# Performance work log

Measured on AMD Instinct MI355X. Metric: run time of the kernel, lower is better.

The kernel has to match this reference:

```python
import jax, jax.numpy as jnp
import numpy as np

BINS = 128
POOL = 4  # AdaptiveAvgPool3d(4) output size


def _resize_axis(a, axis, out_size):
    """1D linear resize along `axis`, matching torch trilinear align_corners=False."""
    in_size = a.shape[axis]
    scale = in_size / out_size
    coords = (jnp.arange(out_size, dtype=a.dtype) + 0.5) * scale - 0.5
    coords = jnp.clip(coords, 0.0, in_size - 1)
    lo = jnp.floor(coords).astype(jnp.int32)
    hi = jnp.minimum(lo + 1, in_size - 1)
    w = coords - lo.astype(a.dtype)
    shape = [1] * a.ndim
    shape[axis] = out_size
    w = w.reshape(shape)
    a_lo = jnp.take(a, lo, axis=axis)
    a_hi = jnp.take(a, hi, axis=axis)
    return a_lo * (1.0 - w) + a_hi * w


def setup_inputs() -> dict:
    key = jax.random.key(0)
    k1, k2, k3 = jax.random.split(key, 3)
    B, C, D, H, W = 2, 64, 64, 64, 64
    Cm = C // 8  # channels // reduction
    x = jax.random.normal(k1, (B, C, D, H, W), jnp.float32)
    w1 = jax.random.normal(k2, (Cm, C), jnp.float32) * 0.1   # Conv3d 1x1, no bias
    w2 = jax.random.normal(k3, (1, Cm), jnp.float32) * 0.1   # Conv3d 1x1, no bias
    return {"x": x, "w1": w1, "w2": w2}


def reference(x, w1, w2):
    B, C, D, H, W = x.shape
    # AdaptiveAvgPool3d(4): D,H,W divisible by 4 -> exact block means
    p = x.reshape(B, C, POOL, D // POOL, POOL, H // POOL, POOL, W // POOL)
    p = p.mean(axis=(3, 5, 7))  # (B, C, 4, 4, 4)
    # 1x1x1 conv == channel contraction
    h = jnp.einsum('oc,bcdhw->bodhw', w1, p)  # (B, Cm, 4, 4, 4)
    # InstanceNorm3d (affine=False), per (B, channel) over spatial dims
    mu = h.mean(axis=(2, 3, 4), keepdims=True)
    var = h.var(axis=(2, 3, 4), keepdims=True)
    h = (h - mu) / jnp.sqrt(var + 1e-5)
    h = jax.nn.gelu(h, approximate=False)  # torch nn.GELU default = exact erf
    s = jax.nn.sigmoid(jnp.einsum('oc,bcdhw->bodhw', w2, h))  # (B, 1, 4, 4, 4)
    # trilinear upsample (align_corners=False), separable per axis
    for axis, size in ((2, D), (3, H), (4, W)):
        s = _resize_axis(s, axis, size)
    weighted = x * s  # broadcast over channels
    x_min = weighted.min()
    x_max = weighted.max()
    x_norm = (weighted - x_min) / (x_max - x_min + 1e-8)
    # torch.histc(bins=BINS, min=0, max=1): values in [0,1]; v==1 -> last bin
    idx = jnp.clip(jnp.floor(x_norm.reshape(-1) * BINS).astype(jnp.int32), 0, BINS - 1)
    hist = jnp.zeros((BINS,), x.dtype).at[idx].add(1.0)
    prob = hist / (hist.sum() + 1e-10)
    entropy = -jnp.sum(prob * jnp.log2(prob + 1e-10))
    return entropy
```

## Files before the change

### kernel.cpp

```cpp
#include <hip/hip_runtime.h>
#include <math.h>

#define BINS 128


__device__ __forceinline__ unsigned mapf(float f) {
    unsigned u = __float_as_uint(f);
    return (u & 0x80000000u) ? ~u : (u | 0x80000000u);
}
__device__ __forceinline__ float unmapf(unsigned m) {
    unsigned u = (m & 0x80000000u) ? (m & 0x7FFFFFFFu) : ~m;
    return __uint_as_float(u);
}
__device__ __forceinline__ float sel4(float g0, float g1, float g2, float g3, int k) {
    float a = (k & 1) ? g1 : g0;
    float b = (k & 1) ? g3 : g2;
    return (k & 2) ? b : a;
}
__device__ __forceinline__ void axgate(int v, int& lo, int& hi, float& fr) {
    float c = ((float)v + 0.5f) * 0.0625f - 0.5f;
    c = fminf(fmaxf(c, 0.0f), 3.0f);
    int l = (int)floorf(c);
    lo = l; hi = min(l + 1, 3); fr = c - (float)l;
}

__global__ __launch_bounds__(256) void pool_kernel(const float* __restrict__ x,
                                                   float* __restrict__ p) {
    const int blk = blockIdx.x;
    const int t = threadIdx.x;
    const float4* xb = (const float4*)x + (size_t)blk * 16384;
    float acc0 = 0.f, acc1 = 0.f, acc2 = 0.f, acc3 = 0.f;
    for (int n = 0; n < 64; n += 4) {
        float4 v0 = xb[(n + 0) * 256 + t]; acc0 += (v0.x + v0.y) + (v0.z + v0.w);
        float4 v1 = xb[(n + 1) * 256 + t]; acc1 += (v1.x + v1.y) + (v1.z + v1.w);
        float4 v2 = xb[(n + 2) * 256 + t]; acc2 += (v2.x + v2.y) + (v2.z + v2.w);
        float4 v3 = xb[(n + 3) * 256 + t]; acc3 += (v3.x + v3.y) + (v3.z + v3.w);
    }
    #pragma unroll
    for (int m = 0; m < 4; ++m) {
        int mask = (m == 0) ? 1 : (m == 1) ? 2 : (m == 2) ? 16 : 32;
        acc0 += __shfl_xor(acc0, mask);
        acc1 += __shfl_xor(acc1, mask);
        acc2 += __shfl_xor(acc2, mask);
        acc3 += __shfl_xor(acc3, mask);
    }
    __shared__ float red[64];
    const int lane = t & 63, wave = t >> 6;
    if (lane < 16 && (lane & 3) == 0) {
        const int pw = lane >> 2;
        red[(0 * 4 + pw) * 4 + wave] = acc0;
        red[(1 * 4 + pw) * 4 + wave] = acc1;
        red[(2 * 4 + pw) * 4 + wave] = acc2;
        red[(3 * 4 + pw) * 4 + wave] = acc3;
    }
    __syncthreads();
    if (t < 16)
        p[blk * 16 + t] = (red[t * 4 + 0] + red[t * 4 + 1] + red[t * 4 + 2] + red[t * 4 + 3]) * (1.0f / 4096.0f);
}

__global__ __launch_bounds__(1024) void mid_kernel(const float* __restrict__ p,
                                                   const float* __restrict__ w1,
                                                   const float* __restrict__ w2,
                                                   float* __restrict__ s_out,
                                                   unsigned* __restrict__ mm,
                                                   unsigned* __restrict__ hist) {
    __shared__ float hs[2 * 8 * 64];
    const int t = threadIdx.x;
    const int b = t >> 9, cm = (t >> 6) & 7, sp = t & 63;
    float h = 0.f;
    const float* pb = p + b * 64 * 64 + sp;
    const float* w1r = w1 + cm * 64;
    for (int c = 0; c < 64; ++c) h += w1r[c] * pb[c * 64];
    float s1 = h;
    #pragma unroll
    for (int m = 1; m <= 32; m <<= 1) s1 += __shfl_xor(s1, m);
    const float mu = s1 * (1.0f / 64.0f);
    float d = h - mu;
    float s2 = d * d;
    #pragma unroll
    for (int m = 1; m <= 32; m <<= 1) s2 += __shfl_xor(s2, m);
    const float var = s2 * (1.0f / 64.0f);
    const float hn = d / sqrtf(var + 1e-5f);
    hs[(b * 8 + cm) * 64 + sp] = 0.5f * hn * (1.0f + erff(hn * 0.70710678118654752440f));
    __syncthreads();
    if (t < 128) {
        const int bb = t >> 6, ss = t & 63;
        float acc = 0.f;
        #pragma unroll
        for (int c = 0; c < 8; ++c) acc += w2[c] * hs[(bb * 8 + c) * 64 + ss];
        s_out[t] = 1.0f / (1.0f + expf(-acc));
    }
    if (t == 0) { mm[0] = 0xFFFFFFFFu; mm[1] = 0u; }
    if (t >= 128 && t < 256) hist[t - 128] = 0u;
}


#define PASS_SETUP2()                                                                 \
    const int t = threadIdx.x;                                                        \
    const int bid = blockIdx.x;                                                       \
    const int cbase = (bid & 7) * 256 + (bid >> 3) * 4;                               \
    const int b = cbase >> 10;                                                        \
    if (t < 64) ls64[t] = s[b * 64 + t];                                              \
    int wl0, wh0, wl1, wh1, wl2, wh2, wl3, wh3;                                       \
    float fw0, fw1, fw2, fw3;                                                         \
    {                                                                                 \
        const int wb = (t & 15) * 4;                                                  \
        axgate(wb + 0, wl0, wh0, fw0); axgate(wb + 1, wl1, wh1, fw1);                 \
        axgate(wb + 2, wl2, wh2, fw2); axgate(wb + 3, wl3, wh3, fw3);                 \
    }                                                                                 \
    const int rbase = t >> 4;                                                         \
    __syncthreads();                                                                  \
    _Pragma("unroll")                                                                 \
    for (int k = 0; k < 4; ++k) {                                                     \
        const int e = k * 256 + t;                                                    \
        const int dloc = e >> 6, hh_ = e & 63;                                        \
        int dl, dh2; float fd; axgate((cbase & 15) * 4 + dloc, dl, dh2, fd);          \
        int hl, hh3; float fh; axgate(hh_, hl, hh3, fh);                              \
        const float w00 = (1.f - fd) * (1.f - fh), w01 = (1.f - fd) * fh;             \
        const float w10 = fd * (1.f - fh), w11 = fd * fh;                             \
        const int i00 = dl * 16 + hl * 4, i01 = dl * 16 + hh3 * 4;                    \
        const int i10 = dh2 * 16 + hl * 4, i11 = dh2 * 16 + hh3 * 4;                  \
        rowg[e] = make_float4(                                                        \
            w00 * ls64[i00 + 0] + w01 * ls64[i01 + 0] + w10 * ls64[i10 + 0] + w11 * ls64[i11 + 0], \
            w00 * ls64[i00 + 1] + w01 * ls64[i01 + 1] + w10 * ls64[i10 + 1] + w11 * ls64[i11 + 1], \
            w00 * ls64[i00 + 2] + w01 * ls64[i01 + 2] + w10 * ls64[i10 + 2] + w11 * ls64[i11 + 2], \
            w00 * ls64[i00 + 3] + w01 * ls64[i01 + 3] + w10 * ls64[i10 + 3] + w11 * ls64[i11 + 3]);\
    }                                                                                 \
    __syncthreads();

#define LOADS16(IT)                                                                   \
    const float4* xp = (const float4*)x + (size_t)(cbase + (IT)) * 4096;              \
    const float4 u0  = xp[ 0*256+t], u1  = xp[ 1*256+t], u2  = xp[ 2*256+t], u3  = xp[ 3*256+t]; \
    const float4 u4  = xp[ 4*256+t], u5  = xp[ 5*256+t], u6  = xp[ 6*256+t], u7  = xp[ 7*256+t]; \
    const float4 u8  = xp[ 8*256+t], u9  = xp[ 9*256+t], u10 = xp[10*256+t], u11 = xp[11*256+t]; \
    const float4 u12 = xp[12*256+t], u13 = xp[13*256+t], u14 = xp[14*256+t], u15 = xp[15*256+t]; \
    __builtin_amdgcn_sched_barrier(0);

#define GATE4A(IT, K, G0, G1, G2, G3)                                                 \
    float G0, G1, G2, G3;                                                             \
    {                                                                                 \
        float4 rg = rowg[(IT) * 256 + (K) * 16 + rbase];                              \
        float lo, hi;                                                                 \
        lo = sel4(rg.x, rg.y, rg.z, rg.w, wl0); hi = sel4(rg.x, rg.y, rg.z, rg.w, wh0); G0 = lo + fw0 * (hi - lo); \
        lo = sel4(rg.x, rg.y, rg.z, rg.w, wl1); hi = sel4(rg.x, rg.y, rg.z, rg.w, wh1); G1 = lo + fw1 * (hi - lo); \
        lo = sel4(rg.x, rg.y, rg.z, rg.w, wl2); hi = sel4(rg.x, rg.y, rg.z, rg.w, wh2); G2 = lo + fw2 * (hi - lo); \
        lo = sel4(rg.x, rg.y, rg.z, rg.w, wl3); hi = sel4(rg.x, rg.y, rg.z, rg.w, wh3); G3 = lo + fw3 * (hi - lo); \
    }

__global__ __launch_bounds__(256) void gated_minmax_kernel(const float* __restrict__ x,
                                                           const float* __restrict__ s,
                                                           unsigned* __restrict__ mm) {
    __shared__ float ls64[64];
    __shared__ float4 rowg[1024];
    __shared__ float red[8];
    PASS_SETUP2()

    float vmin = INFINITY, vmax = -INFINITY;
    #pragma unroll
    for (int it = 0; it < 4; ++it) {
        LOADS16(it)
#define MM1(K, U)                                                                     \
        {                                                                             \
            GATE4A(it, K, g0, g1, g2, g3);                                            \
            float p0 = U.x * g0, p1 = U.y * g1, p2 = U.z * g2, p3 = U.w * g3;         \
            vmin = fminf(vmin, fminf(fminf(p0, p1), fminf(p2, p3)));                  \
            vmax = fmaxf(vmax, fmaxf(fmaxf(p0, p1), fmaxf(p2, p3)));                  \
        }
        MM1(0,u0) MM1(1,u1) MM1(2,u2) MM1(3,u3) MM1(4,u4) MM1(5,u5) MM1(6,u6) MM1(7,u7)
        MM1(8,u8) MM1(9,u9) MM1(10,u10) MM1(11,u11) MM1(12,u12) MM1(13,u13) MM1(14,u14) MM1(15,u15)
#undef MM1
    }

    #pragma unroll
    for (int m = 1; m <= 32; m <<= 1) {
        vmin = fminf(vmin, __shfl_xor(vmin, m));
        vmax = fmaxf(vmax, __shfl_xor(vmax, m));
    }
    const int wave = t >> 6;
    __syncthreads();
    if ((t & 63) == 0) { red[wave] = vmin; red[4 + wave] = vmax; }
    __syncthreads();
    if (t == 0) {
        float m0 = fminf(fminf(red[0], red[1]), fminf(red[2], red[3]));
        float M0 = fmaxf(fmaxf(red[4], red[5]), fmaxf(red[6], red[7]));
        atomicMin(&mm[0], mapf(m0));
        atomicMax(&mm[1], mapf(M0));
    }
}

__global__ __launch_bounds__(256) void gated_hist_kernel(const float* __restrict__ x,
                                                         const float* __restrict__ s,
                                                         const unsigned* __restrict__ mm,
                                                         unsigned* __restrict__ ghist) {
    __shared__ float ls64[64];
    __shared__ float4 rowg[1024];
    __shared__ unsigned lh[BINS];
    if (threadIdx.x < BINS) lh[threadIdx.x] = 0u;
    PASS_SETUP2()

    const float vmin = unmapf(mm[0]);
    const float vmax = unmapf(mm[1]);
    const float inv = 128.0f / (vmax - vmin + 1e-8f);

    #pragma unroll
    for (int it = 0; it < 4; ++it) {
        LOADS16(it)
#define PKK(K, U)                                                                     \
        unsigned pk##K;                                                               \
        {                                                                             \
            GATE4A(it, K, g0, g1, g2, g3);                                            \
            float p0 = U.x * g0, p1 = U.y * g1, p2 = U.z * g2, p3 = U.w * g3;         \
            int i0 = (int)floorf((p0 - vmin) * inv);                                  \
            int i1 = (int)floorf((p1 - vmin) * inv);                                  \
            int i2 = (int)floorf((p2 - vmin) * inv);                                  \
            int i3 = (int)floorf((p3 - vmin) * inv);                                  \
            i0 = min(max(i0, 0), BINS - 1); i1 = min(max(i1, 0), BINS - 1);           \
            i2 = min(max(i2, 0), BINS - 1); i3 = min(max(i3, 0), BINS - 1);           \
            pk##K = (unsigned)i0 | ((unsigned)i1 << 8) |                              \
                    ((unsigned)i2 << 16) | ((unsigned)i3 << 24);                      \
        }
        PKK(0,u0) PKK(1,u1) PKK(2,u2) PKK(3,u3) PKK(4,u4) PKK(5,u5) PKK(6,u6) PKK(7,u7)
        PKK(8,u8) PKK(9,u9) PKK(10,u10) PKK(11,u11) PKK(12,u12) PKK(13,u13) PKK(14,u14) PKK(15,u15)
#undef PKK
        __builtin_amdgcn_sched_barrier(0);
#define AT(K)                                                                         \
        atomicAdd(&lh[pk##K & 255u], 1u);                                             \
        atomicAdd(&lh[(pk##K >> 8) & 255u], 1u);                                      \
        atomicAdd(&lh[(pk##K >> 16) & 255u], 1u);                                     \
        atomicAdd(&lh[pk##K >> 24], 1u);
        AT(0) AT(1) AT(2) AT(3) AT(4) AT(5) AT(6) AT(7)
        AT(8) AT(9) AT(10) AT(11) AT(12) AT(13) AT(14) AT(15)
#undef AT
        __builtin_amdgcn_sched_barrier(0);
    }

    __syncthreads();
    if (t < BINS) {
        unsigned c = lh[t];
        if (c) atomicAdd(&ghist[t], c);
    }
}

__global__ __launch_bounds__(64) void entropy_kernel(const unsigned* __restrict__ ghist,
                                                     float* __restrict__ out) {
    const int t = threadIdx.x;
    float c0 = (float)ghist[t];
    float c1 = (float)ghist[t + 64];
    float s = c0 + c1;
    #pragma unroll
    for (int m = 1; m <= 32; m <<= 1) s += __shfl_xor(s, m);
    const float inv = 1.0f / (s + 1e-10f);
    float p0 = c0 * inv, p1 = c1 * inv;
    float e = p0 * log2f(p0 + 1e-10f) + p1 * log2f(p1 + 1e-10f);
    #pragma unroll
    for (int m = 1; m <= 32; m <<= 1) e += __shfl_xor(e, m);
    if (t == 0) out[0] = -e;
}

extern "C" void kernel_launch(void* const* d_in, const int* in_sizes, int n_in,
                              void* d_out, int out_size, void* d_ws, size_t ws_size,
                              hipStream_t stream) {
    (void)in_sizes; (void)n_in; (void)out_size; (void)ws_size;
    const float* x  = (const float*)d_in[0];
    const float* w1 = (const float*)d_in[1];
    const float* w2 = (const float*)d_in[2];
    float* out = (float*)d_out;
    float* ws  = (float*)d_ws;

    float* p        = ws;
    float* s        = ws + 8192;
    unsigned* mm    = (unsigned*)(ws + 8448);
    unsigned* hist  = (unsigned*)(ws + 8456);

    pool_kernel<<<512, 256, 0, stream>>>(x, p);
    mid_kernel<<<1, 1024, 0, stream>>>(p, w1, w2, s, mm, hist);
    gated_minmax_kernel<<<512, 256, 0, stream>>>(x, s, mm);
    gated_hist_kernel<<<512, 256, 0, stream>>>(x, s, mm, hist);
    entropy_kernel<<<1, 64, 0, stream>>>(hist, out);
}
```

Measured before the change: 96.12 us.

## Fuse min/max, histogram and entropy kernels with a software grid barrier

Merges the gated min/max pass, the histogram pass and the entropy kernel into one persistent 512-block kernel. A global atomic barrier separates the min/max reduction from the histogram phase, and a completion counter lets block 0 compute the entropy. This removes two kernel launches and the repeated per-block gate-table setup. It also replaces the select-based trilinear gate with a 4-weight dot product and folds the bin index into one FMA. The grid barrier assumes all 512 blocks are co-resident, and the FMA index without floor may round differently at bin edges.

```diff
diff --git a/kernel.cpp b/kernel.cpp
--- a/kernel.cpp
+++ b/kernel.cpp
@@ -11,17 +11,28 @@
 __device__ __forceinline__ float unmapf(unsigned m) {
     unsigned u = (m & 0x80000000u) ? (m & 0x7FFFFFFFu) : ~m;
     return __uint_as_float(u);
-}
-__device__ __forceinline__ float sel4(float g0, float g1, float g2, float g3, int k) {
-    float a = (k & 1) ? g1 : g0;
-    float b = (k & 1) ? g3 : g2;
-    return (k & 2) ? b : a;
 }
 __device__ __forceinline__ void axgate(int v, int& lo, int& hi, float& fr) {
     float c = ((float)v + 0.5f) * 0.0625f - 0.5f;
     c = fminf(fmaxf(c, 0.0f), 3.0f);
     int l = (int)floorf(c);
     lo = l; hi = min(l + 1, 3); fr = c - (float)l;
+}
+
+__device__ __forceinline__ void gbar(unsigned* bar, unsigned* gen, unsigned nb) {
+    __syncthreads();
+    if (threadIdx.x == 0) {
+        __threadfence();
+        unsigned g = atomicAdd(gen, 0u);
+        if (atomicAdd(bar, 1u) == nb - 1u) {
+            atomicExch(bar, 0u);
+            __threadfence();
+            atomicAdd(gen, 1u);
+        } else {
+            while (atomicAdd(gen, 0u) == g) __builtin_amdgcn_s_sleep(4);
+        }
+    }
+    __syncthreads();
 }
 
 __global__ __launch_bounds__(256) void pool_kernel(const float* __restrict__ x,
@@ -63,7 +74,8 @@
                                                    const float* __restrict__ w2,
                                                    float* __restrict__ s_out,
                                                    unsigned* __restrict__ mm,
-                                                   unsigned* __restrict__ hist) {
+                                                   unsigned* __restrict__ hist,
+                                                   unsigned* __restrict__ barv) {
     __shared__ float hs[2 * 8 * 64];
     const int t = threadIdx.x;
     const int b = t >> 9, cm = (t >> 6) & 7, sp = t & 63;
@@ -90,42 +102,62 @@
         for (int c = 0; c < 8; ++c) acc += w2[c] * hs[(bb * 8 + c) * 64 + ss];
         s_out[t] = 1.0f / (1.0f + expf(-acc));
     }
-    if (t == 0) { mm[0] = 0xFFFFFFFFu; mm[1] = 0u; }
+    if (t == 0) {
+        mm[0] = 0xFFFFFFFFu; mm[1] = 0u;
+        barv[0] = 0u; barv[1] = 0u; barv[2] = 0u;
+    }
     if (t >= 128 && t < 256) hist[t - 128] = 0u;
 }
 
-
-#define PASS_SETUP2()                                                                 \
-    const int t = threadIdx.x;                                                        \
-    const int bid = blockIdx.x;                                                       \
-    const int cbase = (bid & 7) * 256 + (bid >> 3) * 4;                               \
-    const int b = cbase >> 10;                                                        \
-    if (t < 64) ls64[t] = s[b * 64 + t];                                              \
-    int wl0, wh0, wl1, wh1, wl2, wh2, wl3, wh3;                                       \
-    float fw0, fw1, fw2, fw3;                                                         \
-    {                                                                                 \
-        const int wb = (t & 15) * 4;                                                  \
-        axgate(wb + 0, wl0, wh0, fw0); axgate(wb + 1, wl1, wh1, fw1);                 \
-        axgate(wb + 2, wl2, wh2, fw2); axgate(wb + 3, wl3, wh3, fw3);                 \
-    }                                                                                 \
-    const int rbase = t >> 4;                                                         \
-    __syncthreads();                                                                  \
-    _Pragma("unroll")                                                                 \
-    for (int k = 0; k < 4; ++k) {                                                     \
-        const int e = k * 256 + t;                                                    \
-        const int dloc = e >> 6, hh_ = e & 63;                                        \
-        int dl, dh2; float fd; axgate((cbase & 15) * 4 + dloc, dl, dh2, fd);          \
-        int hl, hh3; float fh; axgate(hh_, hl, hh3, fh);                              \
-        const float w00 = (1.f - fd) * (1.f - fh), w01 = (1.f - fd) * fh;             \
-        const float w10 = fd * (1.f - fh), w11 = fd * fh;                             \
-        const int i00 = dl * 16 + hl * 4, i01 = dl * 16 + hh3 * 4;                    \
-        const int i10 = dh2 * 16 + hl * 4, i11 = dh2 * 16 + hh3 * 4;                  \
-        rowg[e] = make_float4(                                                        \
-            w00 * ls64[i00 + 0] + w01 * ls64[i01 + 0] + w10 * ls64[i10 + 0] + w11 * ls64[i11 + 0], \
-            w00 * ls64[i00 + 1] + w01 * ls64[i01 + 1] + w10 * ls64[i10 + 1] + w11 * ls64[i11 + 1], \
-            w00 * ls64[i00 + 2] + w01 * ls64[i01 + 2] + w10 * ls64[i10 + 2] + w11 * ls64[i11 + 2], \
-            w00 * ls64[i00 + 3] + w01 * ls64[i01 + 3] + w10 * ls64[i10 + 3] + w11 * ls64[i11 + 3]);\
-    }                                                                                 \
+__global__ __launch_bounds__(256) void fused_mmh_kernel(const float* __restrict__ x,
+                                                        const float* __restrict__ s,
+                                                        unsigned* __restrict__ mm,
+                                                        unsigned* __restrict__ ghist,
+                                                        unsigned* __restrict__ barv,
+                                                        float* __restrict__ out) {
+    __shared__ float ls64[64];
+    __shared__ float4 rowg[1024];
+    __shared__ unsigned lh[BINS];
+    __shared__ float red[8];
+    const int t = threadIdx.x;
+    const int bid = blockIdx.x;
+    const int cbase = (bid & 7) * 256 + (bid >> 3) * 4;
+    const int b = cbase >> 10;
+    if (t < 64) ls64[t] = s[b * 64 + t];
+    if (t < BINS) lh[t] = 0u;
+
+    float4 wva, wvb, wvc, wvd;
+    {
+        const int wb = (t & 15) * 4;
+        #define MKWV(WV, J)                                                           \
+        {                                                                             \
+            int lo, hi; float fr; axgate(wb + (J), lo, hi, fr);                       \
+            const float om = 1.0f - fr;                                               \
+            WV.x = (lo == 0 ? om : 0.f) + (hi == 0 ? fr : 0.f);                       \
+            WV.y = (lo == 1 ? om : 0.f) + (hi == 1 ? fr : 0.f);                       \
+            WV.z = (lo == 2 ? om : 0.f) + (hi == 2 ? fr : 0.f);                       \
+            WV.w = (lo == 3 ? om : 0.f) + (hi == 3 ? fr : 0.f);                       \
+        }
+        MKWV(wva, 0) MKWV(wvb, 1) MKWV(wvc, 2) MKWV(wvd, 3)
+        #undef MKWV
+    }
+    const int rbase = t >> 4;
+    __syncthreads();
+    #pragma unroll
+    for (int k = 0; k < 4; ++k) {
+        const int e = k * 256 + t;
+        int dl, dh2; float fd; axgate((cbase & 15) * 4 + (e >> 6), dl, dh2, fd);
+        int hl, hh3; float fh; axgate(e & 63, hl, hh3, fh);
+        const float w00 = (1.f - fd) * (1.f - fh), w01 = (1.f - fd) * fh;
+        const float w10 = fd * (1.f - fh), w11 = fd * fh;
+        const int i00 = dl * 16 + hl * 4, i01 = dl * 16 + hh3 * 4;
+        const int i10 = dh2 * 16 + hl * 4, i11 = dh2 * 16 + hh3 * 4;
+        rowg[e] = make_float4(
+            w00 * ls64[i00 + 0] + w01 * ls64[i01 + 0] + w10 * ls64[i10 + 0] + w11 * ls64[i11 + 0],
+            w00 * ls64[i00 + 1] + w01 * ls64[i01 + 1] + w10 * ls64[i10 + 1] + w11 * ls64[i11 + 1],
+            w00 * ls64[i00 + 2] + w01 * ls64[i01 + 2] + w10 * ls64[i10 + 2] + w11 * ls64[i11 + 2],
+            w00 * ls64[i00 + 3] + w01 * ls64[i01 + 3] + w10 * ls64[i10 + 3] + w11 * ls64[i11 + 3]);
+    }
     __syncthreads();
 
 #define LOADS16(IT)                                                                   \
@@ -136,71 +168,59 @@
     const float4 u12 = xp[12*256+t], u13 = xp[13*256+t], u14 = xp[14*256+t], u15 = xp[15*256+t]; \
     __builtin_amdgcn_sched_barrier(0);
 
-#define GATE4A(IT, K, G0, G1, G2, G3)                                                 \
+#define GATE4W(IT, K, G0, G1, G2, G3)                                                 \
     float G0, G1, G2, G3;                                                             \
     {                                                                                 \
         float4 rg = rowg[(IT) * 256 + (K) * 16 + rbase];                              \
-        float lo, hi;                                                                 \
-        lo = sel4(rg.x, rg.y, rg.z, rg.w, wl0); hi = sel4(rg.x, rg.y, rg.z, rg.w, wh0); G0 = lo + fw0 * (hi - lo); \
-        lo = sel4(rg.x, rg.y, rg.z, rg.w, wl1); hi = sel4(rg.x, rg.y, rg.z, rg.w, wh1); G1 = lo + fw1 * (hi - lo); \
-        lo = sel4(rg.x, rg.y, rg.z, rg.w, wl2); hi = sel4(rg.x, rg.y, rg.z, rg.w, wh2); G2 = lo + fw2 * (hi - lo); \
-        lo = sel4(rg.x, rg.y, rg.z, rg.w, wl3); hi = sel4(rg.x, rg.y, rg.z, rg.w, wh3); G3 = lo + fw3 * (hi - lo); \
-    }
-
-__global__ __launch_bounds__(256) void gated_minmax_kernel(const float* __restrict__ x,
-                                                           const float* __restrict__ s,
-                                                           unsigned* __restrict__ mm) {
-    __shared__ float ls64[64];
-    __shared__ float4 rowg[1024];
-    __shared__ float red[8];
-    PASS_SETUP2()
-
-    float vmin = INFINITY, vmax = -INFINITY;
-    #pragma unroll
-    for (int it = 0; it < 4; ++it) {
-        LOADS16(it)
+        G0 = rg.x * wva.x + rg.y * wva.y + rg.z * wva.z + rg.w * wva.w;               \
+        G1 = rg.x * wvb.x + rg.y * wvb.y + rg.z * wvb.z + rg.w * wvb.w;               \
+        G2 = rg.x * wvc.x + rg.y * wvc.y + rg.z * wvc.z + rg.w * wvc.w;               \
+        G3 = rg.x * wvd.x + rg.y * wvd.y + rg.z * wvd.z + rg.w * wvd.w;               \
+    }
+
+    {
+        float vmin = INFINITY, vmax = -INFINITY;
+        #pragma unroll
+        for (int it = 0; it < 4; ++it) {
+            LOADS16(it)
 #define MM1(K, U)                                                                     \
-        {                                                                             \
-            GATE4A(it, K, g0, g1, g2, g3);                                            \
-            float p0 = U.x * g0, p1 = U.y * g1, p2 = U.z * g2, p3 = U.w * g3;         \
-            vmin = fminf(vmin, fminf(fminf(p0, p1), fminf(p2, p3)));                  \
-            vmax = fmaxf(vmax, fmaxf(fmaxf(p0, p1), fmaxf(p2, p3)));                  \
-        }
-        MM1(0,u0) MM1(1,u1) MM1(2,u2) MM1(3,u3) MM1(4,u4) MM1(5,u5) MM1(6,u6) MM1(7,u7)
-        MM1(8,u8) MM1(9,u9) MM1(10,u10) MM1(11,u11) MM1(12,u12) MM1(13,u13) MM1(14,u14) MM1(15,u15)
+            {                                                                         \
+                GATE4W(it, K, g0, g1, g2, g3);                                        \
+                float p0 = U.x * g0, p1 = U.y * g1, p2 = U.z * g2, p3 = U.w * g3;     \
+                vmin = fminf(vmin, fminf(fminf(p0, p1), fminf(p2, p3)));              \
+                vmax = fmaxf(vmax, fmaxf(fmaxf(p0, p1), fmaxf(p2, p3)));              \
+            }
+            MM1(0,u0) MM1(1,u1) MM1(2,u2) MM1(3,u3) MM1(4,u4) MM1(5,u5) MM1(6,u6) MM1(7,u7)
+            MM1(8,u8) MM1(9,u9) MM1(10,u10) MM1(11,u11) MM1(12,u12) MM1(13,u13) MM1(14,u14) MM1(15,u15)
 #undef MM1
-    }
-
-    #pragma unroll
-    for (int m = 1; m <= 32; m <<= 1) {
-        vmin = fminf(vmin, __shfl_xor(vmin, m));
-        vmax = fmaxf(vmax, __shfl_xor(vmax, m));
-    }
-    const int wave = t >> 6;
-    __syncthreads();
-    if ((t & 63) == 0) { red[wave] = vmin; red[4 + wave] = vmax; }
-    __syncthreads();
+        }
+        #pragma unroll
+        for (int m = 1; m <= 32; m <<= 1) {
+            vmin = fminf(vmin, __shfl_xor(vmin, m));
+            vmax = fmaxf(vmax, __shfl_xor(vmax, m));
+        }
+        const int wave = t >> 6;
+        __syncthreads();
+        if ((t & 63) == 0) { red[wave] = vmin; red[4 + wave] = vmax; }
+        __syncthreads();
+        if (t == 0) {
+            float m0 = fminf(fminf(red[0], red[1]), fminf(red[2], red[3]));
+            float M0 = fmaxf(fmaxf(red[4], red[5]), fmaxf(red[6], red[7]));
+            atomicMin(&mm[0], mapf(m0));
+            atomicMax(&mm[1], mapf(M0));
+        }
+    }
+
+    gbar(&barv[0], &barv[1], 512u);
+
     if (t == 0) {
-        float m0 = fminf(fminf(red[0], red[1]), fminf(red[2], red[3]));
-        float M0 = fmaxf(fmaxf(red[4], red[5]), fmaxf(red[6], red[7]));
-        atomicMin(&mm[0], mapf(m0));
-        atomicMax(&mm[1], mapf(M0));
-    }
-}
-
-__global__ __launch_bounds__(256) void gated_hist_kernel(const float* __restrict__ x,
-                                                         const float* __restrict__ s,
-                                                         const unsigned* __restrict__ mm,
-                                                         unsigned* __restrict__ ghist) {
-    __shared__ float ls64[64];
-    __shared__ float4 rowg[1024];
-    __shared__ unsigned lh[BINS];
-    if (threadIdx.x < BINS) lh[threadIdx.x] = 0u;
-    PASS_SETUP2()
-
-    const float vmin = unmapf(mm[0]);
-    const float vmax = unmapf(mm[1]);
-    const float inv = 128.0f / (vmax - vmin + 1e-8f);
+        red[0] = unmapf(atomicAdd(&mm[0], 0u));
+        red[1] = unmapf(atomicAdd(&mm[1], 0u));
+    }
+    __syncthreads();
+    const float vmn = red[0];
+    const float inv = 128.0f / (red[1] - vmn + 1e-8f);
+    const float nvm = -vmn * inv;
 
     #pragma unroll
     for (int it = 0; it < 4; ++it) {
@@ -208,12 +228,12 @@
 #define PKK(K, U)                                                                     \
         unsigned pk##K;                                                               \
         {                                                                             \
-            GATE4A(it, K, g0, g1, g2, g3);                                            \
+            GATE4W(it, K, g0, g1, g2, g3);                                            \
             float p0 = U.x * g0, p1 = U.y * g1, p2 = U.z * g2, p3 = U.w * g3;         \
-            int i0 = (int)floorf((p0 - vmin) * inv);                                  \
-            int i1 = (int)floorf((p1 - vmin) * inv);                                  \
-            int i2 = (int)floorf((p2 - vmin) * inv);                                  \
-            int i3 = (int)floorf((p3 - vmin) * inv);                                  \
+            int i0 = (int)(p0 * inv + nvm);                                           \
+            int i1 = (int)(p1 * inv + nvm);                                           \
+            int i2 = (int)(p2 * inv + nvm);                                           \
+            int i3 = (int)(p3 * inv + nvm);                                           \
             i0 = min(max(i0, 0), BINS - 1); i1 = min(max(i1, 0), BINS - 1);           \
             i2 = min(max(i2, 0), BINS - 1); i3 = min(max(i3, 0), BINS - 1);           \
             pk##K = (unsigned)i0 | ((unsigned)i1 << 8) |                              \
@@ -233,28 +253,35 @@
 #undef AT
         __builtin_amdgcn_sched_barrier(0);
     }
-
     __syncthreads();
     if (t < BINS) {
         unsigned c = lh[t];
         if (c) atomicAdd(&ghist[t], c);
     }
-}
-
-__global__ __launch_bounds__(64) void entropy_kernel(const unsigned* __restrict__ ghist,
-                                                     float* __restrict__ out) {
-    const int t = threadIdx.x;
-    float c0 = (float)ghist[t];
-    float c1 = (float)ghist[t + 64];
-    float s = c0 + c1;
-    #pragma unroll
-    for (int m = 1; m <= 32; m <<= 1) s += __shfl_xor(s, m);
-    const float inv = 1.0f / (s + 1e-10f);
-    float p0 = c0 * inv, p1 = c1 * inv;
-    float e = p0 * log2f(p0 + 1e-10f) + p1 * log2f(p1 + 1e-10f);
-    #pragma unroll
-    for (int m = 1; m <= 32; m <<= 1) e += __shfl_xor(e, m);
-    if (t == 0) out[0] = -e;
+    __syncthreads();
+    if (t == 0) { __threadfence(); atomicAdd(&barv[2], 1u); }
+
+    if (bid == 0) {
+        if (t == 0) {
+            while (atomicAdd(&barv[2], 0u) < 512u) __builtin_amdgcn_s_sleep(4);
+        }
+        __syncthreads();
+        if (t < 64) {
+            float c0 = (float)atomicAdd(&ghist[t], 0u);
+            float c1 = (float)atomicAdd(&ghist[t + 64], 0u);
+            float ssum = c0 + c1;
+            #pragma unroll
+            for (int m = 1; m <= 32; m <<= 1) ssum += __shfl_xor(ssum, m);
+            const float is = 1.0f / (ssum + 1e-10f);
+            float p0 = c0 * is, p1 = c1 * is;
+            float e = p0 * log2f(p0 + 1e-10f) + p1 * log2f(p1 + 1e-10f);
+            #pragma unroll
+            for (int m = 1; m <= 32; m <<= 1) e += __shfl_xor(e, m);
+            if (t == 0) out[0] = -e;
+        }
+    }
+#undef LOADS16
+#undef GATE4W
 }
 
 extern "C" void kernel_launch(void* const* d_in, const int* in_sizes, int n_in,
@@ -270,11 +297,10 @@
     float* p        = ws;
     float* s        = ws + 8192;
     unsigned* mm    = (unsigned*)(ws + 8448);
+    unsigned* barv  = (unsigned*)(ws + 8450);
     unsigned* hist  = (unsigned*)(ws + 8456);
 
     pool_kernel<<<512, 256, 0, stream>>>(x, p);
-    mid_kernel<<<1, 1024, 0, stream>>>(p, w1, w2, s, mm, hist);
-    gated_minmax_kernel<<<512, 256, 0, stream>>>(x, s, mm);
-    gated_hist_kernel<<<512, 256, 0, stream>>>(x, s, mm, hist);
-    entropy_kernel<<<1, 64, 0, stream>>>(hist, out);
-}
+    mid_kernel<<<1, 1024, 0, stream>>>(p, w1, w2, s, mm, hist, barv);
+    fused_mmh_kernel<<<512, 256, 0, stream>>>(x, s, mm, hist, barv, out);
+}
```

Measured after the change: 152.6 us. 1.59x slower.

## Replace select-based W-gate interpolation with weight dot products and simplify streaming loops

Applied to the files above, without the earlier changes.

The per-thread W-axis interpolation now uses precomputed 4-wide weight vectors and a dot product instead of sel4 selects and a lerp. The 16-load batched blocks with sched_barriers are replaced by a single 64-iteration loop unrolled by 4, leaving load scheduling to the compiler. In the histogram pass the bin index becomes a fused multiply-add with truncation instead of a subtract, multiply and floorf, and atomics are issued right after each element. Fewer loads in flight could reduce memory-level parallelism, and truncation differs from floor for slightly negative values, but the clamp to zero covers that.

```diff
diff --git a/kernel.cpp b/kernel.cpp
--- a/kernel.cpp
+++ b/kernel.cpp
@@ -11,11 +11,6 @@
 __device__ __forceinline__ float unmapf(unsigned m) {
     unsigned u = (m & 0x80000000u) ? (m & 0x7FFFFFFFu) : ~m;
     return __uint_as_float(u);
-}
-__device__ __forceinline__ float sel4(float g0, float g1, float g2, float g3, int k) {
-    float a = (k & 1) ? g1 : g0;
-    float b = (k & 1) ? g3 : g2;
-    return (k & 2) ? b : a;
 }
 __device__ __forceinline__ void axgate(int v, int& lo, int& hi, float& fr) {
     float c = ((float)v + 0.5f) * 0.0625f - 0.5f;
@@ -95,27 +90,36 @@
 }
 
 
-#define PASS_SETUP2()                                                                 \
+#define PASS_SETUP4()                                                                 \
     const int t = threadIdx.x;                                                        \
     const int bid = blockIdx.x;                                                       \
     const int cbase = (bid & 7) * 256 + (bid >> 3) * 4;                               \
     const int b = cbase >> 10;                                                        \
     if (t < 64) ls64[t] = s[b * 64 + t];                                              \
-    int wl0, wh0, wl1, wh1, wl2, wh2, wl3, wh3;                                       \
-    float fw0, fw1, fw2, fw3;                                                         \
+    float4 wva, wvb, wvc, wvd;      \
     {                                                                                 \
         const int wb = (t & 15) * 4;                                                  \
-        axgate(wb + 0, wl0, wh0, fw0); axgate(wb + 1, wl1, wh1, fw1);                 \
-        axgate(wb + 2, wl2, wh2, fw2); axgate(wb + 3, wl3, wh3, fw3);                 \
+        int lo, hi; float fr, om;                                                     \
+        axgate(wb + 0, lo, hi, fr); om = 1.0f - fr;                                   \
+        wva = make_float4((lo==0?om:0.f)+(hi==0?fr:0.f), (lo==1?om:0.f)+(hi==1?fr:0.f),\
+                          (lo==2?om:0.f)+(hi==2?fr:0.f), (lo==3?om:0.f)+(hi==3?fr:0.f));\
+        axgate(wb + 1, lo, hi, fr); om = 1.0f - fr;                                   \
+        wvb = make_float4((lo==0?om:0.f)+(hi==0?fr:0.f), (lo==1?om:0.f)+(hi==1?fr:0.f),\
+                          (lo==2?om:0.f)+(hi==2?fr:0.f), (lo==3?om:0.f)+(hi==3?fr:0.f));\
+        axgate(wb + 2, lo, hi, fr); om = 1.0f - fr;                                   \
+        wvc = make_float4((lo==0?om:0.f)+(hi==0?fr:0.f), (lo==1?om:0.f)+(hi==1?fr:0.f),\
+                          (lo==2?om:0.f)+(hi==2?fr:0.f), (lo==3?om:0.f)+(hi==3?fr:0.f));\
+        axgate(wb + 3, lo, hi, fr); om = 1.0f - fr;                                   \
+        wvd = make_float4((lo==0?om:0.f)+(hi==0?fr:0.f), (lo==1?om:0.f)+(hi==1?fr:0.f),\
+                          (lo==2?om:0.f)+(hi==2?fr:0.f), (lo==3?om:0.f)+(hi==3?fr:0.f));\
     }                                                                                 \
     const int rbase = t >> 4;                                                         \
     __syncthreads();                                                                  \
     _Pragma("unroll")                                                                 \
-    for (int k = 0; k < 4; ++k) {                                                     \
+    for (int k = 0; k < 4; ++k) {             \
         const int e = k * 256 + t;                                                    \
-        const int dloc = e >> 6, hh_ = e & 63;                                        \
-        int dl, dh2; float fd; axgate((cbase & 15) * 4 + dloc, dl, dh2, fd);          \
-        int hl, hh3; float fh; axgate(hh_, hl, hh3, fh);                              \
+        int dl, dh2; float fd; axgate((cbase & 15) * 4 + (e >> 6), dl, dh2, fd);      \
+        int hl, hh3; float fh; axgate(e & 63, hl, hh3, fh);                           \
         const float w00 = (1.f - fd) * (1.f - fh), w01 = (1.f - fd) * fh;             \
         const float w10 = fd * (1.f - fh), w11 = fd * fh;                             \
         const int i00 = dl * 16 + hl * 4, i01 = dl * 16 + hh3 * 4;                    \
@@ -126,25 +130,17 @@
             w00 * ls64[i00 + 2] + w01 * ls64[i01 + 2] + w10 * ls64[i10 + 2] + w11 * ls64[i11 + 2], \
             w00 * ls64[i00 + 3] + w01 * ls64[i01 + 3] + w10 * ls64[i10 + 3] + w11 * ls64[i11 + 3]);\
     }                                                                                 \
-    __syncthreads();
-
-#define LOADS16(IT)                                                                   \
-    const float4* xp = (const float4*)x + (size_t)(cbase + (IT)) * 4096;              \
-    const float4 u0  = xp[ 0*256+t], u1  = xp[ 1*256+t], u2  = xp[ 2*256+t], u3  = xp[ 3*256+t]; \
-    const float4 u4  = xp[ 4*256+t], u5  = xp[ 5*256+t], u6  = xp[ 6*256+t], u7  = xp[ 7*256+t]; \
-    const float4 u8  = xp[ 8*256+t], u9  = xp[ 9*256+t], u10 = xp[10*256+t], u11 = xp[11*256+t]; \
-    const float4 u12 = xp[12*256+t], u13 = xp[13*256+t], u14 = xp[14*256+t], u15 = xp[15*256+t]; \
-    __builtin_amdgcn_sched_barrier(0);
-
-#define GATE4A(IT, K, G0, G1, G2, G3)                                                 \
+    __syncthreads();                                                                  \
+    const float4* xp = (const float4*)x + (size_t)cbase * 4096 + t;
+
+#define GATE4R(K, G0, G1, G2, G3)                                                     \
     float G0, G1, G2, G3;                                                             \
     {                                                                                 \
-        float4 rg = rowg[(IT) * 256 + (K) * 16 + rbase];                              \
-        float lo, hi;                                                                 \
-        lo = sel4(rg.x, rg.y, rg.z, rg.w, wl0); hi = sel4(rg.x, rg.y, rg.z, rg.w, wh0); G0 = lo + fw0 * (hi - lo); \
-        lo = sel4(rg.x, rg.y, rg.z, rg.w, wl1); hi = sel4(rg.x, rg.y, rg.z, rg.w, wh1); G1 = lo + fw1 * (hi - lo); \
-        lo = sel4(rg.x, rg.y, rg.z, rg.w, wl2); hi = sel4(rg.x, rg.y, rg.z, rg.w, wh2); G2 = lo + fw2 * (hi - lo); \
-        lo = sel4(rg.x, rg.y, rg.z, rg.w, wl3); hi = sel4(rg.x, rg.y, rg.z, rg.w, wh3); G3 = lo + fw3 * (hi - lo); \
+        float4 rg = rowg[(((K) >> 4) << 8) + (((K) & 15) << 4) + rbase];              \
+        G0 = rg.x * wva.x + rg.y * wva.y + rg.z * wva.z + rg.w * wva.w;               \
+        G1 = rg.x * wvb.x + rg.y * wvb.y + rg.z * wvb.z + rg.w * wvb.w;               \
+        G2 = rg.x * wvc.x + rg.y * wvc.y + rg.z * wvc.z + rg.w * wvc.w;               \
+        G3 = rg.x * wvd.x + rg.y * wvd.y + rg.z * wvd.z + rg.w * wvd.w;               \
     }
 
 __global__ __launch_bounds__(256) void gated_minmax_kernel(const float* __restrict__ x,
@@ -153,22 +149,16 @@
     __shared__ float ls64[64];
     __shared__ float4 rowg[1024];
     __shared__ float red[8];
-    PASS_SETUP2()
+    PASS_SETUP4()
 
     float vmin = INFINITY, vmax = -INFINITY;
-    #pragma unroll
-    for (int it = 0; it < 4; ++it) {
-        LOADS16(it)
-#define MM1(K, U)                                                                     \
-        {                                                                             \
-            GATE4A(it, K, g0, g1, g2, g3);                                            \
-            float p0 = U.x * g0, p1 = U.y * g1, p2 = U.z * g2, p3 = U.w * g3;         \
-            vmin = fminf(vmin, fminf(fminf(p0, p1), fminf(p2, p3)));                  \
-            vmax = fmaxf(vmax, fmaxf(fmaxf(p0, p1), fmaxf(p2, p3)));                  \
-        }
-        MM1(0,u0) MM1(1,u1) MM1(2,u2) MM1(3,u3) MM1(4,u4) MM1(5,u5) MM1(6,u6) MM1(7,u7)
-        MM1(8,u8) MM1(9,u9) MM1(10,u10) MM1(11,u11) MM1(12,u12) MM1(13,u13) MM1(14,u14) MM1(15,u15)
-#undef MM1
+    #pragma unroll 4
+    for (int k = 0; k < 64; ++k) {
+        float4 u = xp[k * 256];
+        GATE4R(k, g0, g1, g2, g3);
+        float p0 = u.x * g0, p1 = u.y * g1, p2 = u.z * g2, p3 = u.w * g3;
+        vmin = fminf(vmin, fminf(fminf(p0, p1), fminf(p2, p3)));
+        vmax = fmaxf(vmax, fmaxf(fmaxf(p0, p1), fmaxf(p2, p3)));
     }
 
     #pragma unroll
@@ -196,42 +186,27 @@
     __shared__ float4 rowg[1024];
     __shared__ unsigned lh[BINS];
     if (threadIdx.x < BINS) lh[threadIdx.x] = 0u;
-    PASS_SETUP2()
-
-    const float vmin = unmapf(mm[0]);
-    const float vmax = unmapf(mm[1]);
-    const float inv = 128.0f / (vmax - vmin + 1e-8f);
-
-    #pragma unroll
-    for (int it = 0; it < 4; ++it) {
-        LOADS16(it)
-#define PKK(K, U)                                                                     \
-        unsigned pk##K;                                                               \
-        {                                                                             \
-            GATE4A(it, K, g0, g1, g2, g3);                                            \
-            float p0 = U.x * g0, p1 = U.y * g1, p2 = U.z * g2, p3 = U.w * g3;         \
-            int i0 = (int)floorf((p0 - vmin) * inv);                                  \
-            int i1 = (int)floorf((p1 - vmin) * inv);                                  \
-            int i2 = (int)floorf((p2 - vmin) * inv);                                  \
-            int i3 = (int)floorf((p3 - vmin) * inv);                                  \
-            i0 = min(max(i0, 0), BINS - 1); i1 = min(max(i1, 0), BINS - 1);           \
-            i2 = min(max(i2, 0), BINS - 1); i3 = min(max(i3, 0), BINS - 1);           \
-            pk##K = (unsigned)i0 | ((unsigned)i1 << 8) |                              \
-                    ((unsigned)i2 << 16) | ((unsigned)i3 << 24);                      \
-        }
-        PKK(0,u0) PKK(1,u1) PKK(2,u2) PKK(3,u3) PKK(4,u4) PKK(5,u5) PKK(6,u6) PKK(7,u7)
-        PKK(8,u8) PKK(9,u9) PKK(10,u10) PKK(11,u11) PKK(12,u12) PKK(13,u13) PKK(14,u14) PKK(15,u15)
-#undef PKK
-        __builtin_amdgcn_sched_barrier(0);
-#define AT(K)                                                                         \
-        atomicAdd(&lh[pk##K & 255u], 1u);                                             \
-        atomicAdd(&lh[(pk##K >> 8) & 255u], 1u);                                      \
-        atomicAdd(&lh[(pk##K >> 16) & 255u], 1u);                                     \
-        atomicAdd(&lh[pk##K >> 24], 1u);
-        AT(0) AT(1) AT(2) AT(3) AT(4) AT(5) AT(6) AT(7)
-        AT(8) AT(9) AT(10) AT(11) AT(12) AT(13) AT(14) AT(15)
-#undef AT
-        __builtin_amdgcn_sched_barrier(0);
+    PASS_SETUP4()
+
+    const float vmn = unmapf(mm[0]);
+    const float inv = 128.0f / (unmapf(mm[1]) - vmn + 1e-8f);
+    const float nvm = -vmn * inv;
+
+    #pragma unroll 4
+    for (int k = 0; k < 64; ++k) {
+        float4 u = xp[k * 256];
+        GATE4R(k, g0, g1, g2, g3);
+        float p0 = u.x * g0, p1 = u.y * g1, p2 = u.z * g2, p3 = u.w * g3;
+        int i0 = (int)(p0 * inv + nvm);
+        int i1 = (int)(p1 * inv + nvm);
+        int i2 = (int)(p2 * inv + nvm);
+        int i3 = (int)(p3 * inv + nvm);
+        i0 = min(max(i0, 0), BINS - 1); i1 = min(max(i1, 0), BINS - 1);
+        i2 = min(max(i2, 0), BINS - 1); i3 = min(max(i3, 0), BINS - 1);
+        atomicAdd(&lh[i0], 1u);
+        atomicAdd(&lh[i1], 1u);
+        atomicAdd(&lh[i2], 1u);
+        atomicAdd(&lh[i3], 1u);
     }
 
     __syncthreads();
```

Result: slower. 98.36 us (+2.3%).
